# Kernel optimization log

Hardware: AMD Instinct MI355X
Metric: run time of the kernel (lower is better)

## Reference

```python
import jax, jax.numpy as jnp
import numpy as np

N_G, N_D, D = 50000, 50000, 64
R, L, NNZ, B = 32, 2, 1600000, 2048
TEMP, LAMBDA_1, LAMBDA_2, DROPOUT = 0.2, 0.2, 1e-7, 0.1


def setup_inputs() -> dict:
    key = jax.random.key(0)
    ks = jax.random.split(key, 14)
    uids = jax.random.randint(ks[0], (B,), 0, N_G)
    iids = jax.random.randint(ks[1], (B,), 0, N_D)
    pos = jax.random.randint(ks[2], (B,), 0, N_D)
    neg = jax.random.randint(ks[3], (B,), 0, N_D)
    E_g_0 = jax.random.normal(ks[4], (N_G, D), jnp.float32) * 0.01
    E_d_0 = jax.random.normal(ks[5], (N_D, D), jnp.float32) * 0.01
    rows = jax.random.randint(ks[6], (NNZ,), 0, N_G)
    cols = jax.random.randint(ks[7], (NNZ,), 0, N_D)
    vals = jax.random.uniform(ks[8], (NNZ,), jnp.float32)
    g_mul_s = jax.random.normal(ks[9], (N_G, R), jnp.float32) * 0.1
    v_mul_s = jax.random.normal(ks[10], (N_D, R), jnp.float32) * 0.1
    ut = jax.random.normal(ks[11], (R, N_G), jnp.float32) * (N_G ** -0.5)
    vt = jax.random.normal(ks[12], (R, N_D), jnp.float32) * (N_D ** -0.5)
    drop_u = jax.random.uniform(ks[13], (L, 2, NNZ), jnp.float32)
    return {"uids": uids, "iids": iids, "pos": pos, "neg": neg,
            "E_g_0": E_g_0, "E_d_0": E_d_0, "rows": rows, "cols": cols,
            "vals": vals, "g_mul_s": g_mul_s, "v_mul_s": v_mul_s,
            "ut": ut, "vt": vt, "drop_u": drop_u}


def reference(uids, iids, pos, neg, E_g_0, E_d_0, rows, cols, vals,
              g_mul_s, v_mul_s, ut, vt, drop_u):
    # sparse_dropout keep masks (independent per layer and per spmm call)
    keep = (drop_u > DROPOUT).astype(vals.dtype) / (1.0 - DROPOUT)  # [L,2,NNZ]
    E_g, E_d = E_g_0, E_d_0
    E_g_sum, E_d_sum = E_g_0, E_d_0
    G_g_sum, G_d_sum = E_g_0, E_d_0
    for layer in range(L):
        # Z_g = dropout(A) @ E_d ; Z_d = dropout(A).T @ E_g  (COO spmm)
        vg = vals * keep[layer, 0]
        Z_g = jax.ops.segment_sum(vg[:, None] * E_d[cols], rows, num_segments=N_G)
        vd = vals * keep[layer, 1]
        Z_d = jax.ops.segment_sum(vd[:, None] * E_g[rows], cols, num_segments=N_D)
        # low-rank SVD branch
        G_g = g_mul_s @ (vt @ E_d)  # [n_g, d]
        G_d = v_mul_s @ (ut @ E_g)  # [n_d, d]
        E_g, E_d = Z_g, Z_d
        E_g_sum = E_g_sum + E_g
        E_d_sum = E_d_sum + E_d
        G_g_sum = G_g_sum + G_g
        G_d_sum = G_d_sum + G_d
    # InfoNCE-style contrastive loss (exactly as torch: log(sum exp + eps))
    S_g = (G_g_sum[uids] @ E_g_sum.T) / TEMP  # [B, n_g]
    S_d = (G_d_sum[iids] @ E_d_sum.T) / TEMP  # [B, n_d]
    neg_score = jnp.log(jnp.exp(S_g).sum(1) + 1e-8).mean() \
              + jnp.log(jnp.exp(S_d).sum(1) + 1e-8).mean()
    pos_score = jnp.clip((G_g_sum[uids] * E_g_sum[uids]).sum(1) / TEMP, -5.0, 5.0).mean() \
              + jnp.clip((G_d_sum[iids] * E_d_sum[iids]).sum(1) / TEMP, -5.0, 5.0).mean()
    loss_s = -pos_score + neg_score
    # BPR loss
    g_emb = E_g_sum[uids]
    diff = (g_emb * E_d_sum[pos]).sum(-1) - (g_emb * E_d_sum[neg]).sum(-1)
    loss_r = -jnp.log(jax.nn.sigmoid(diff)).mean()
    # L2 reg over trainable embedding params
    loss_reg = LAMBDA_2 * (jnp.sum(E_g_0 ** 2) + jnp.sum(E_d_0 ** 2))
    loss = loss_r + LAMBDA_1 * loss_s + loss_reg
    return (loss, loss_r, LAMBDA_1 * loss_s)
```

## Files before the change

### kernel.cpp

```cpp
#include <hip/hip_runtime.h>
#include <hip/hip_bf16.h>
#include <math.h>

#define N_Gc 50000
#define N_Dc 50000
#define DIM 64
#define RNK 32
#define NNZc 1600000
#define BSZ 2048
#define KEEPV (1.0f/0.9f)
#define INVT 5.0f
#define NBK2 196
#define NBLK 200
#define NSL 48
#define EPB 8000
#define MCH 256
#define MBLK 196

typedef __attribute__((ext_vector_type(8))) short bfrag;
typedef __attribute__((ext_vector_type(4))) float f32x4;
typedef unsigned long long u64;

__device__ inline ushort f2bf(float f) {
  union { float f; unsigned int u; } v; v.f = f;
  unsigned int r = (v.u + 0x7fffu + ((v.u >> 16) & 1u)) >> 16;
  return (ushort)r;
}
__device__ inline float bf2f(ushort u) {
  union { unsigned int i; float f; } v; v.i = ((unsigned int)u) << 16;
  return v.f;
}

__global__ __launch_bounds__(256) void hist3_kernel(const int* __restrict__ rows, const int* __restrict__ cols,
                                                    int* __restrict__ cntR, int* __restrict__ cntC) {
  __shared__ int lh_r[NBK2];
  __shared__ int lh_c[NBK2];
  int t = threadIdx.x, blk = blockIdx.x;
  if (t < NBK2) { lh_r[t] = 0; lh_c[t] = 0; }
  __syncthreads();
  int e0 = blk*EPB;
  for (int i = e0 + t; i < e0 + EPB; i += 256) {
    atomicAdd(&lh_r[__builtin_nontemporal_load(&rows[i]) >> 8], 1);
    atomicAdd(&lh_c[__builtin_nontemporal_load(&cols[i]) >> 8], 1);
  }
  __syncthreads();
  if (t < NBK2) {
    cntR[t*NBLK + blk] = lh_r[t];
    cntC[t*NBLK + blk] = lh_c[t];
  }
}

__global__ __launch_bounds__(1024) void cscan2_kernel(const int* __restrict__ cntA, int* __restrict__ cbA, int* __restrict__ bpA,
                                                      const int* __restrict__ cntB, int* __restrict__ cbB, int* __restrict__ bpB) {
  const int n = NBK2*NBLK;
  const int* cnt = blockIdx.x ? cntB : cntA;
  int* cb = blockIdx.x ? cbB : cbA;
  int* bp = blockIdx.x ? bpB : bpA;
  __shared__ int wsum[16];
  int t = threadIdx.x, lane = t & 63, w = t >> 6;
  int carry = 0;
  for (int base = 0; base < n; base += 1024) {
    int i = base + t;
    int v = (i < n) ? cnt[i] : 0;
    int x = v;
    #pragma unroll
    for (int o = 1; o < 64; o <<= 1) { int y = __shfl_up(x, o); if (lane >= o) x += y; }
    if (lane == 63) wsum[w] = x;
    __syncthreads();
    if (t < 16) {
      int s = wsum[t];
      #pragma unroll
      for (int o = 1; o < 16; o <<= 1) { int y = __shfl_up(s, o); if (t >= o) s += y; }
      wsum[t] = s;
    }
    __syncthreads();
    int wpre = (w == 0) ? 0 : wsum[w-1];
    int total = wsum[15];
    int ex = carry + wpre + (x - v);
    if (i < n) {
      cb[i] = ex;
      if (i % NBLK == 0) bp[i/NBLK] = ex;
    }
    carry += total;
    __syncthreads();
  }
  if (t == 0) bp[NBK2] = carry;
}

__global__ __launch_bounds__(256) void phaseA2_kernel(const int* __restrict__ rows, const int* __restrict__ cols,
    const float* __restrict__ vals, const float* __restrict__ drop,
    const int* __restrict__ cbR, const int* __restrict__ cbC,
    u64* __restrict__ stage_r, u64* __restrict__ stage_c) {
  __shared__ int cnt_r[NBK2], cnt_c[NBK2];
  __shared__ int base_r[NBK2], base_c[NBK2];
  int t = threadIdx.x, blk = blockIdx.x;
  if (t < NBK2) {
    cnt_r[t] = 0; cnt_c[t] = 0;
    base_r[t] = cbR[t*NBLK + blk];
    base_c[t] = cbC[t*NBLK + blk];
  }
  __syncthreads();
  int e0 = blk*EPB;
  for (int i = e0 + t; i < e0 + EPB; i += 256) {
    int r = __builtin_nontemporal_load(&rows[i]);
    int c = __builtin_nontemporal_load(&cols[i]);
    u64 vb = (u64)__float_as_uint(__builtin_nontemporal_load(&vals[i])) << 32;
    unsigned int dr0 = (__builtin_nontemporal_load(&drop[i]) > 0.1f) ? (1u<<24) : 0u;
    unsigned int dc0 = (__builtin_nontemporal_load(&drop[(size_t)NNZc + i]) > 0.1f) ? (1u<<24) : 0u;
    unsigned int dr1 = (__builtin_nontemporal_load(&drop[2*(size_t)NNZc + i]) > 0.1f) ? (1u<<25) : 0u;
    unsigned int dc1 = (__builtin_nontemporal_load(&drop[3*(size_t)NNZc + i]) > 0.1f) ? (1u<<25) : 0u;
    int br = r >> 8, bc = c >> 8;
    int p = base_r[br] + atomicAdd(&cnt_r[br], 1);
    stage_r[p] = vb | (unsigned int)c | ((unsigned int)(r & 255) << 16) | dr0 | dr1;
    int q = base_c[bc] + atomicAdd(&cnt_c[bc], 1);
    stage_c[q] = vb | (unsigned int)r | ((unsigned int)(c & 255) << 16) | dc0 | dc1;
  }
}

__global__ __launch_bounds__(256) void phaseB2_kernel(
    const int* __restrict__ bptrR, int* __restrict__ ptroutR, const u64* __restrict__ stageR,
    ushort* __restrict__ fcolR, float* __restrict__ fw0R, float* __restrict__ fw1R,
    const int* __restrict__ bptrC, int* __restrict__ ptroutC, const u64* __restrict__ stageC,
    ushort* __restrict__ fcolC, float* __restrict__ fw0C, float* __restrict__ fw1C, int n) {
  const int side = blockIdx.y;
  const int* bptr = side ? bptrC : bptrR;
  int* ptrout = side ? ptroutC : ptroutR;
  const u64* stage = side ? stageC : stageR;
  ushort* fcol = side ? fcolC : fcolR;
  float* fw0 = side ? fw0C : fw0R;
  float* fw1 = side ? fw1C : fw1R;
  __shared__ int cnt[256];
  __shared__ int pos[256];
  __shared__ int woff[4];
  int t = threadIdx.x, b = blockIdx.x;
  int base_row = b*256;
  int base = bptr[b], endp = bptr[b+1];
  cnt[t] = 0;
  __syncthreads();
  for (int k = base + t; k < endp; k += 256) {
    unsigned int lo = (unsigned int)__builtin_nontemporal_load(&stage[k]);
    atomicAdd(&cnt[(lo >> 16) & 255], 1);
  }
  __syncthreads();
  int lane = t & 63, w = t >> 6;
  int c = cnt[t], x = c;
  #pragma unroll
  for (int o = 1; o < 64; o <<= 1) { int y = __shfl_up(x, o); if (lane >= o) x += y; }
  if (lane == 63) woff[w] = x;
  __syncthreads();
  if (t == 0) { woff[1] += woff[0]; woff[2] += woff[1]; woff[3] += woff[2]; }
  __syncthreads();
  int excl = ((w == 0) ? 0 : woff[w-1]) + (x - c);
  pos[t] = excl;
  int rr = base_row + t;
  if (rr <= n) ptrout[rr] = base + excl;
  __syncthreads();
  for (int k = base + t; k < endp; k += 256) {
    u64 rec = __builtin_nontemporal_load(&stage[k]);
    unsigned int lo = (unsigned int)rec;
    int rel = (lo >> 16) & 255;
    int p = base + atomicAdd(&pos[rel], 1);
    float v = __uint_as_float((unsigned int)(rec >> 32));
    fcol[p] = (ushort)(lo & 0xffffu);
    fw0[p] = (lo & (1u<<24)) ? v*KEEPV : 0.f;
    fw1[p] = (lo & (1u<<25)) ? v*KEEPV : 0.f;
  }
}

__device__ __forceinline__ float spmm_row(const ushort* __restrict__ fcol, const float* __restrict__ fw,
                                          const ushort* __restrict__ Eb, int k0, int end, int lane) {
  float acc = 0.f;
  int nfull = (end - k0) >> 3;
  int cc[8]; float ww[8];
  if (nfull > 0) {
    #pragma unroll
    for (int u = 0; u < 8; u++) {
      cc[u] = __builtin_nontemporal_load(&fcol[k0+u]);
      ww[u] = __builtin_nontemporal_load(&fw[k0+u]);
    }
    for (int b = 1; b < nfull; b++) {
      int kn = k0 + b*8;
      int cn[8]; float wn[8];
      #pragma unroll
      for (int u = 0; u < 8; u++) {
        cn[u] = __builtin_nontemporal_load(&fcol[kn+u]);
        wn[u] = __builtin_nontemporal_load(&fw[kn+u]);
      }
      #pragma unroll
      for (int u = 0; u < 8; u++) acc += ww[u]*bf2f(Eb[(size_t)cc[u]*DIM + lane]);
      #pragma unroll
      for (int u = 0; u < 8; u++) { cc[u] = cn[u]; ww[u] = wn[u]; }
    }
    #pragma unroll
    for (int u = 0; u < 8; u++) acc += ww[u]*bf2f(Eb[(size_t)cc[u]*DIM + lane]);
  }
  for (int k = k0 + nfull*8; k < end; k++)
    acc += __builtin_nontemporal_load(&fw[k])*bf2f(Eb[(size_t)__builtin_nontemporal_load(&fcol[k])*DIM + lane]);
  return acc;
}

__global__ __launch_bounds__(256) void spmm_l0_kernel(
    const int* __restrict__ ptrR, const ushort* __restrict__ fcolR, const float* __restrict__ fwR,
    const ushort* __restrict__ EbR, ushort* __restrict__ ZbR,
    const int* __restrict__ ptrC, const ushort* __restrict__ fcolC, const float* __restrict__ fwC,
    const ushort* __restrict__ EbC, ushort* __restrict__ ZbC, int nrows) {
  const int side = blockIdx.y;
  const int* ptr = side ? ptrC : ptrR;
  const ushort* fcol = side ? fcolC : fcolR;
  const float* fw = side ? fwC : fwR;
  const ushort* Eb = side ? EbC : EbR;
  ushort* Zb = side ? ZbC : ZbR;
  int lane = threadIdx.x & 63;
  int row = blockIdx.x*4 + (threadIdx.x >> 6);
  if (row >= nrows) return;
  float acc = spmm_row(fcol, fw, Eb, ptr[row], ptr[row+1], lane);
  Zb[(size_t)row*DIM + lane] = f2bf(acc);
}

__global__ __launch_bounds__(256) void spmm_l1_kernel(
    const int* __restrict__ ptrR, const ushort* __restrict__ fcolR, const float* __restrict__ fwR,
    const ushort* __restrict__ ZbOR, const float* __restrict__ E0R, const ushort* __restrict__ ZbSR,
    ushort* __restrict__ EoutR,
    const int* __restrict__ ptrC, const ushort* __restrict__ fcolC, const float* __restrict__ fwC,
    const ushort* __restrict__ ZbOC, const float* __restrict__ E0C, const ushort* __restrict__ ZbSC,
    ushort* __restrict__ EoutC, int nrows) {
  const int side = blockIdx.y;
  const int* ptr = side ? ptrC : ptrR;
  const ushort* fcol = side ? fcolC : fcolR;
  const float* fw = side ? fwC : fwR;
  const ushort* ZbO = side ? ZbOC : ZbOR;
  const float* E0 = side ? E0C : E0R;
  const ushort* ZbS = side ? ZbSC : ZbSR;
  ushort* Eout = side ? EoutC : EoutR;
  int lane = threadIdx.x & 63;
  int row = blockIdx.x*4 + (threadIdx.x >> 6);
  if (row >= nrows) return;
  float acc = spmm_row(fcol, fw, ZbO, ptr[row], ptr[row+1], lane);
  size_t o = (size_t)row*DIM + lane;
  acc += __builtin_nontemporal_load(&E0[o]) + bf2f(ZbS[o]);
  Eout[o] = f2bf(acc);
}

__global__ __launch_bounds__(256) void matred2_kernel(
    const float* __restrict__ vrowA, const float* __restrict__ E0A, const ushort* __restrict__ ZbA, float* __restrict__ MpA,
    const float* __restrict__ vrowB, const float* __restrict__ E0B, const ushort* __restrict__ ZbB, float* __restrict__ MpB,
    int n) {
  const int side = blockIdx.y;
  const float* vrow = side ? vrowB : vrowA;
  const float* E0 = side ? E0B : E0A;
  const ushort* Zb = side ? ZbB : ZbA;
  float* Mpart = side ? MpB : MpA;
  __shared__ float vs[RNK*MCH];
  __shared__ float part[RNK*DIM];
  int t = threadIdx.x, lane = t & 63, w = t >> 6;
  int ci0 = blockIdx.x*MCH;
  int cnt = min(MCH, n - ci0);
  for (int idx = t; idx < RNK*DIM; idx += 256) part[idx] = 0.f;
  for (int idx = t; idx < RNK*MCH; idx += 256) {
    int r = idx >> 8, i = idx & (MCH-1);
    vs[idx] = (i < cnt) ? __builtin_nontemporal_load(&vrow[(size_t)r*n + ci0 + i]) : 0.f;
  }
  __syncthreads();
  float acc[RNK];
  #pragma unroll
  for (int r = 0; r < RNK; r++) acc[r] = 0.f;
  int iw0 = w*64;
  for (int ii = 0; ii < 64; ii += 4) {
    int i = iw0 + ii;
    int gi = ci0 + i;
    float x0 = 0.f, x1 = 0.f, x2 = 0.f, x3 = 0.f;
    if (i+0 < cnt) x0 = E0[(size_t)(gi+0)*DIM + lane] + bf2f(Zb[(size_t)(gi+0)*DIM + lane]);
    if (i+1 < cnt) x1 = E0[(size_t)(gi+1)*DIM + lane] + bf2f(Zb[(size_t)(gi+1)*DIM + lane]);
    if (i+2 < cnt) x2 = E0[(size_t)(gi+2)*DIM + lane] + bf2f(Zb[(size_t)(gi+2)*DIM + lane]);
    if (i+3 < cnt) x3 = E0[(size_t)(gi+3)*DIM + lane] + bf2f(Zb[(size_t)(gi+3)*DIM + lane]);
    #pragma unroll
    for (int r = 0; r < RNK; r++) {
      float4 v4 = *(const float4*)&vs[r*MCH + i];
      acc[r] += v4.x*x0 + v4.y*x1 + v4.z*x2 + v4.w*x3;
    }
  }
  #pragma unroll
  for (int r = 0; r < RNK; r++) atomicAdd(&part[r*DIM + lane], acc[r]);
  __syncthreads();
  float* dst = Mpart + (size_t)blockIdx.x*(RNK*DIM);
  for (int idx = t; idx < RNK*DIM; idx += 256) dst[idx] = part[idx];
}

__global__ __launch_bounds__(256) void mreduce_kernel(const float* __restrict__ MpA, float* __restrict__ MA,
                                                      const float* __restrict__ MpB, float* __restrict__ MB, int nblk) {
  const float* Mpart = blockIdx.y ? MpB : MpA;
  float* M = blockIdx.y ? MB : MA;
  int idx = blockIdx.x*256 + threadIdx.x;
  if (idx < RNK*DIM) {
    float s = 0.f;
    for (int b = 0; b < nblk; b++) s += Mpart[(size_t)b*(RNK*DIM) + idx];
    M[idx] = s;
  }
}

__global__ __launch_bounds__(256) void gsmall_kernel(
    const int* __restrict__ idsA, const float* __restrict__ E0A, const float* __restrict__ mulA,
    const float* __restrict__ MA, float* __restrict__ outA, ushort* __restrict__ outbA,
    const int* __restrict__ idsB, const float* __restrict__ E0B, const float* __restrict__ mulB,
    const float* __restrict__ MB, float* __restrict__ outB, ushort* __restrict__ outbB) {
  const int side = blockIdx.y;
  const int* ids = side ? idsB : idsA;
  const float* E0 = side ? E0B : E0A;
  const float* mul = side ? mulB : mulA;
  const float* M = side ? MB : MA;
  float* out = side ? outB : outA;
  ushort* outb = side ? outbB : outbA;
  __shared__ float Ms[RNK*DIM];
  int t = threadIdx.x;
  for (int i = t; i < RNK*DIM; i += 256) Ms[i] = M[i];
  __syncthreads();
  int b = blockIdx.x*4 + (t >> 6), lane = t & 63;
  int u = ids[b];
  float a = E0[(size_t)u*DIM + lane];
  #pragma unroll
  for (int r = 0; r < RNK; r++) a += mul[(size_t)u*RNK + r]*Ms[r*DIM + lane];
  out[(size_t)b*DIM + lane] = a;
  outb[(size_t)b*DIM + lane] = f2bf(a);
}

__global__ __launch_bounds__(256) void convsq_kernel(const float* __restrict__ inA, ushort* __restrict__ outA,
                                                     const float* __restrict__ inB, ushort* __restrict__ outB,
                                                     int n4, float* __restrict__ acc) {
  const float* in = blockIdx.y ? inB : inA;
  ushort* out = blockIdx.y ? outB : outA;
  __shared__ float ls[4];
  int t = threadIdx.x;
  int idx = blockIdx.x*256 + t;
  int stride = gridDim.x*256;
  float s = 0.f;
  for (int i = idx; i < n4; i += stride) {
    float4 v = *(const float4*)&in[(size_t)i*4];
    ushort4 o;
    o.x = f2bf(v.x); o.y = f2bf(v.y); o.z = f2bf(v.z); o.w = f2bf(v.w);
    *(ushort4*)&out[(size_t)i*4] = o;
    s += v.x*v.x + v.y*v.y + v.z*v.z + v.w*v.w;
  }
  #pragma unroll
  for (int o = 32; o > 0; o >>= 1) s += __shfl_xor(s, o);
  if ((t & 63) == 0) ls[t >> 6] = s;
  __syncthreads();
  if (t == 0) atomicAdd(acc, ls[0] + ls[1] + ls[2] + ls[3]);
}

__global__ __launch_bounds__(256) void lse_mfma_kernel(
    const ushort* __restrict__ Ag, const ushort* __restrict__ Xg, float* __restrict__ seg,
    const ushort* __restrict__ Ad, const ushort* __restrict__ Xd, float* __restrict__ sed,
    int nj) {
  const ushort* A = blockIdx.y ? Ad : Ag;
  const ushort* X = blockIdx.y ? Xd : Xg;
  float* sumexp = blockIdx.y ? sed : seg;
  __shared__ __align__(16) ushort Xs[64*68];
  int t = threadIdx.x, lane = t & 63, w = t >> 6;
  int bt = blockIdx.x & 31, js = blockIdx.x >> 5;
  int b0 = bt*64;
  int m = lane & 15, q = lane >> 4;
  const ushort* Arow = A + (size_t)(b0 + w*16 + m)*DIM + q*8;
  bfrag a0 = *(const bfrag*)(Arow);
  bfrag a1 = *(const bfrag*)(Arow + 32);
  float rs0 = 0.f, rs1 = 0.f, rs2 = 0.f, rs3 = 0.f;
  int njt = (nj + 63) >> 6;
  for (int jt = js; jt < njt; jt += NSL) {
    int j0 = jt << 6;
    __syncthreads();
    for (int c = t; c < 512; c += 256) {
      int r = c >> 3, k8 = (c & 7) << 3;
      int j = j0 + r;
      ushort4 v0 = {0,0,0,0}, v1 = {0,0,0,0};
      if (j < nj) {
        const ushort4* src = (const ushort4*)(X + (size_t)j*DIM + k8);
        v0 = src[0]; v1 = src[1];
      }
      *(ushort4*)&Xs[r*68 + k8]     = v0;
      *(ushort4*)&Xs[r*68 + k8 + 4] = v1;
    }
    __syncthreads();
    #pragma unroll
    for (int jq = 0; jq < 4; jq++) {
      int jr = jq*16 + m;
      union { bfrag f; uint2 u2[2]; } B0, B1;
      B0.u2[0] = *(const uint2*)&Xs[jr*68 + q*8];
      B0.u2[1] = *(const uint2*)&Xs[jr*68 + q*8 + 4];
      B1.u2[0] = *(const uint2*)&Xs[jr*68 + 32 + q*8];
      B1.u2[1] = *(const uint2*)&Xs[jr*68 + 32 + q*8 + 4];
      f32x4 acc = {0.f, 0.f, 0.f, 0.f};
      acc = __builtin_amdgcn_mfma_f32_16x16x32_bf16(a0, B0.f, acc, 0, 0, 0);
      acc = __builtin_amdgcn_mfma_f32_16x16x32_bf16(a1, B1.f, acc, 0, 0, 0);
      int jg = j0 + jr;
      if (jg < nj) {
        rs0 += __expf(acc[0]*INVT);
        rs1 += __expf(acc[1]*INVT);
        rs2 += __expf(acc[2]*INVT);
        rs3 += __expf(acc[3]*INVT);
      }
    }
  }
  #pragma unroll
  for (int o = 1; o < 16; o <<= 1) {
    rs0 += __shfl_xor(rs0, o);
    rs1 += __shfl_xor(rs1, o);
    rs2 += __shfl_xor(rs2, o);
    rs3 += __shfl_xor(rs3, o);
  }
  if (m == 0) {
    float* dst = &sumexp[b0 + w*16 + q*4];
    atomicAdd(&dst[0], rs0);
    atomicAdd(&dst[1], rs1);
    atomicAdd(&dst[2], rs2);
    atomicAdd(&dst[3], rs3);
  }
}

__global__ __launch_bounds__(256) void perb_kernel(const int* __restrict__ uids, const int* __restrict__ iids,
    const int* __restrict__ pos, const int* __restrict__ neg,
    const float* __restrict__ Ggu, const float* __restrict__ Gdi,
    const ushort* __restrict__ Egs_b, const ushort* __restrict__ Eds_b,
    const float* __restrict__ seg, const float* __restrict__ sed,
    float* __restrict__ accs) {
  __shared__ float lsum[3][4];
  int t = threadIdx.x, lane = t & 63, w = t >> 6;
  int b = blockIdx.x*4 + w;
  int u = uids[b], it = iids[b], p = pos[b], ng = neg[b];
  float egu = bf2f(Egs_b[(size_t)u*DIM + lane]);
  float d1 = Ggu[(size_t)b*DIM + lane]*egu;
  float d2 = Gdi[(size_t)b*DIM + lane]*bf2f(Eds_b[(size_t)it*DIM + lane]);
  float d3 = egu*bf2f(Eds_b[(size_t)p*DIM + lane]);
  float d4 = egu*bf2f(Eds_b[(size_t)ng*DIM + lane]);
  #pragma unroll
  for (int o = 32; o > 0; o >>= 1) {
    d1 += __shfl_xor(d1, o);
    d2 += __shfl_xor(d2, o);
    d3 += __shfl_xor(d3, o);
    d4 += __shfl_xor(d4, o);
  }
  if (lane == 0) {
    float pterm = fminf(fmaxf(d1*INVT, -5.f), 5.f) + fminf(fmaxf(d2*INVT, -5.f), 5.f);
    float diff = d3 - d4;
    lsum[0][w] = pterm;
    lsum[1][w] = log1pf(expf(-diff));
    lsum[2][w] = logf(seg[b] + 1e-8f) + logf(sed[b] + 1e-8f);
  }
  __syncthreads();
  if (t < 3) atomicAdd(&accs[t], lsum[t][0] + lsum[t][1] + lsum[t][2] + lsum[t][3]);
}

__global__ void final_kernel(const float* __restrict__ accs, float* __restrict__ out) {
  float posm = accs[0]*(1.f/BSZ);
  float lr   = accs[1]*(1.f/BSZ);
  float negm = accs[2]*(1.f/BSZ);
  float reg  = 1e-7f*accs[3];
  float l1ls = 0.2f*(negm - posm);
  out[0] = lr + l1ls + reg;
  out[1] = lr;
  out[2] = l1ls;
}

extern "C" void kernel_launch(void* const* d_in, const int* in_sizes, int n_in,
                              void* d_out, int out_size, void* d_ws, size_t ws_size,
                              hipStream_t stream) {
  (void)in_sizes; (void)n_in; (void)out_size;
  const int*   uids = (const int*)d_in[0];
  const int*   iids = (const int*)d_in[1];
  const int*   pos  = (const int*)d_in[2];
  const int*   neg  = (const int*)d_in[3];
  const float* Eg0  = (const float*)d_in[4];
  const float* Ed0  = (const float*)d_in[5];
  const int*   rows = (const int*)d_in[6];
  const int*   cols = (const int*)d_in[7];
  const float* vals = (const float*)d_in[8];
  const float* gms  = (const float*)d_in[9];
  const float* vms  = (const float*)d_in[10];
  const float* ut   = (const float*)d_in[11];
  const float* vt   = (const float*)d_in[12];
  const float* drop = (const float*)d_in[13];
  float* out = (float*)d_out;

  float* ws = (float*)d_ws;
  const size_t ED = (size_t)N_Gc*DIM;
  float* REG_A = ws;
  float* REG_B = REG_A + ED;
  int* ptr_r = (int*)(REG_B + ED);
  int* ptr_c = ptr_r + (N_Gc + 1);
  int* bptr_r = ptr_c + (N_Dc + 1);
  int* bptr_c = bptr_r + (NBK2 + 1);
  int* cntR = bptr_c + (NBK2 + 1);
  int* cntC = cntR + NBK2*NBLK;
  int* cbR  = cntC + NBK2*NBLK;
  int* cbC  = cbR + NBK2*NBLK;
  ushort* fcol_r = (ushort*)(cbC + NBK2*NBLK);
  float* fw_r0  = (float*)(fcol_r + NNZc);
  float* fw_r1  = fw_r0 + NNZc;
  ushort* fcol_c = (ushort*)(fw_r1 + NNZc);
  float* fw_c0  = (float*)(fcol_c + NNZc);
  float* fw_c1  = fw_c0 + NNZc;
  float* Ggu = fw_c1 + NNZc;
  float* Gdi = Ggu + (size_t)BSZ*DIM;
  ushort* Ggu_b = (ushort*)(Gdi + (size_t)BSZ*DIM);
  ushort* Gdi_b = Ggu_b + (size_t)BSZ*DIM;
  float* Mg  = (float*)(Gdi_b + (size_t)BSZ*DIM);
  float* Md  = Mg + RNK*DIM;
  float* seg = Md + RNK*DIM;
  float* sed = seg + BSZ;
  float* accs = sed + BSZ;
  float* MpG = accs + 16;
  float* MpD = MpG + (size_t)MBLK*RNK*DIM;

  u64* stage_r = (u64*)REG_A;
  u64* stage_c = (u64*)REG_B;
  ushort* Zg0_b = (ushort*)REG_A;
  ushort* Zd0_b = Zg0_b + ED;
  ushort* Eg0_b = (ushort*)REG_B;
  ushort* Ed0_b = Eg0_b + ED;
  ushort* Egs_b = (ushort*)REG_B;
  ushort* Eds_b = Egs_b + ED;

  size_t need = ((char*)(MpD + (size_t)MBLK*RNK*DIM)) - ((char*)d_ws);
  if (ws_size < need) return;

  hipMemsetAsync(seg, 0, sizeof(float)*(2*BSZ + 16), stream);

  hist3_kernel<<<NBLK, 256, 0, stream>>>(rows, cols, cntR, cntC);
  cscan2_kernel<<<2, 1024, 0, stream>>>(cntR, cbR, bptr_r, cntC, cbC, bptr_c);
  phaseA2_kernel<<<NBLK, 256, 0, stream>>>(rows, cols, vals, drop, cbR, cbC, stage_r, stage_c);
  phaseB2_kernel<<<dim3(NBK2, 2), 256, 0, stream>>>(
      bptr_r, ptr_r, stage_r, fcol_r, fw_r0, fw_r1,
      bptr_c, ptr_c, stage_c, fcol_c, fw_c0, fw_c1, N_Gc);

  int n4 = (int)(ED/4);
  convsq_kernel<<<dim3(1024, 2), 256, 0, stream>>>(Eg0, Eg0_b, Ed0, Ed0_b, n4, accs + 3);

  int spmm_blocks = (N_Gc + 3)/4;
  spmm_l0_kernel<<<dim3(spmm_blocks, 2), 256, 0, stream>>>(
      ptr_r, fcol_r, fw_r0, Ed0_b, Zg0_b,
      ptr_c, fcol_c, fw_c0, Eg0_b, Zd0_b, N_Gc);
  spmm_l1_kernel<<<dim3(spmm_blocks, 2), 256, 0, stream>>>(
      ptr_r, fcol_r, fw_r1, Zd0_b, Eg0, Zg0_b, Egs_b,
      ptr_c, fcol_c, fw_c1, Zg0_b, Ed0, Zd0_b, Eds_b, N_Gc);

  matred2_kernel<<<dim3(MBLK, 2), 256, 0, stream>>>(
      vt, Ed0, Zd0_b, MpG,
      ut, Eg0, Zg0_b, MpD, N_Dc);
  mreduce_kernel<<<dim3((RNK*DIM + 255)/256, 2), 256, 0, stream>>>(MpG, Mg, MpD, Md, MBLK);

  gsmall_kernel<<<dim3(BSZ/4, 2), 256, 0, stream>>>(
      uids, Eg0, gms, Mg, Ggu, Ggu_b,
      iids, Ed0, vms, Md, Gdi, Gdi_b);

  lse_mfma_kernel<<<dim3(32*NSL, 2), 256, 0, stream>>>(Ggu_b, Egs_b, seg, Gdi_b, Eds_b, sed, N_Gc);

  perb_kernel<<<BSZ/4, 256, 0, stream>>>(uids, iids, pos, neg, Ggu, Gdi, Egs_b, Eds_b, seg, sed, accs);
  final_kernel<<<1, 1, 0, stream>>>(accs, out);
}
```

Before: 707.6 us.

## Halve sort buckets to 128 rows and stage bucket sort in shared memory

Bucket width for the two-pass COO-to-CSR radix sort drops from 256 to 128 rows, giving 391 buckets and twice as many phase-B blocks. Phase B now scatters each bucket's records into an LDS buffer of up to 6144 entries, then writes the sorted output with coalesced, contiguous stores. A global-scatter fallback handles oversized buckets. The goal is to replace random global writes with coalesced ones and raise parallelism, at the cost of 48KB of LDS per block, which limits occupancy, and a larger histogram and scan.

```diff
diff --git a/kernel.cpp b/kernel.cpp
--- a/kernel.cpp
+++ b/kernel.cpp
@@ -10,12 +10,13 @@
 #define BSZ 2048
 #define KEEPV (1.0f/0.9f)
 #define INVT 5.0f
-#define NBK2 196
+#define NBK3 391
 #define NBLK 200
 #define NSL 48
 #define EPB 8000
 #define MCH 256
 #define MBLK 196
+#define SCAP 6144
 
 typedef __attribute__((ext_vector_type(8))) short bfrag;
 typedef __attribute__((ext_vector_type(4))) float f32x4;
@@ -33,26 +34,26 @@
 
 __global__ __launch_bounds__(256) void hist3_kernel(const int* __restrict__ rows, const int* __restrict__ cols,
                                                     int* __restrict__ cntR, int* __restrict__ cntC) {
-  __shared__ int lh_r[NBK2];
-  __shared__ int lh_c[NBK2];
+  __shared__ int lh_r[NBK3];
+  __shared__ int lh_c[NBK3];
   int t = threadIdx.x, blk = blockIdx.x;
-  if (t < NBK2) { lh_r[t] = 0; lh_c[t] = 0; }
+  for (int j = t; j < NBK3; j += 256) { lh_r[j] = 0; lh_c[j] = 0; }
   __syncthreads();
   int e0 = blk*EPB;
   for (int i = e0 + t; i < e0 + EPB; i += 256) {
-    atomicAdd(&lh_r[__builtin_nontemporal_load(&rows[i]) >> 8], 1);
-    atomicAdd(&lh_c[__builtin_nontemporal_load(&cols[i]) >> 8], 1);
-  }
-  __syncthreads();
-  if (t < NBK2) {
-    cntR[t*NBLK + blk] = lh_r[t];
-    cntC[t*NBLK + blk] = lh_c[t];
+    atomicAdd(&lh_r[__builtin_nontemporal_load(&rows[i]) >> 7], 1);
+    atomicAdd(&lh_c[__builtin_nontemporal_load(&cols[i]) >> 7], 1);
+  }
+  __syncthreads();
+  for (int j = t; j < NBK3; j += 256) {
+    cntR[j*NBLK + blk] = lh_r[j];
+    cntC[j*NBLK + blk] = lh_c[j];
   }
 }
 
 __global__ __launch_bounds__(1024) void cscan2_kernel(const int* __restrict__ cntA, int* __restrict__ cbA, int* __restrict__ bpA,
                                                       const int* __restrict__ cntB, int* __restrict__ cbB, int* __restrict__ bpB) {
-  const int n = NBK2*NBLK;
+  const int n = NBK3*NBLK;
   const int* cnt = blockIdx.x ? cntB : cntA;
   int* cb = blockIdx.x ? cbB : cbA;
   int* bp = blockIdx.x ? bpB : bpA;
@@ -84,20 +85,20 @@
     carry += total;
     __syncthreads();
   }
-  if (t == 0) bp[NBK2] = carry;
+  if (t == 0) bp[NBK3] = carry;
 }
 
 __global__ __launch_bounds__(256) void phaseA2_kernel(const int* __restrict__ rows, const int* __restrict__ cols,
     const float* __restrict__ vals, const float* __restrict__ drop,
     const int* __restrict__ cbR, const int* __restrict__ cbC,
     u64* __restrict__ stage_r, u64* __restrict__ stage_c) {
-  __shared__ int cnt_r[NBK2], cnt_c[NBK2];
-  __shared__ int base_r[NBK2], base_c[NBK2];
+  __shared__ int cnt_r[NBK3], cnt_c[NBK3];
+  __shared__ int base_r[NBK3], base_c[NBK3];
   int t = threadIdx.x, blk = blockIdx.x;
-  if (t < NBK2) {
-    cnt_r[t] = 0; cnt_c[t] = 0;
-    base_r[t] = cbR[t*NBLK + blk];
-    base_c[t] = cbC[t*NBLK + blk];
+  for (int j = t; j < NBK3; j += 256) {
+    cnt_r[j] = 0; cnt_c[j] = 0;
+    base_r[j] = cbR[j*NBLK + blk];
+    base_c[j] = cbC[j*NBLK + blk];
   }
   __syncthreads();
   int e0 = blk*EPB;
@@ -109,15 +110,15 @@
     unsigned int dc0 = (__builtin_nontemporal_load(&drop[(size_t)NNZc + i]) > 0.1f) ? (1u<<24) : 0u;
     unsigned int dr1 = (__builtin_nontemporal_load(&drop[2*(size_t)NNZc + i]) > 0.1f) ? (1u<<25) : 0u;
     unsigned int dc1 = (__builtin_nontemporal_load(&drop[3*(size_t)NNZc + i]) > 0.1f) ? (1u<<25) : 0u;
-    int br = r >> 8, bc = c >> 8;
+    int br = r >> 7, bc = c >> 7;
     int p = base_r[br] + atomicAdd(&cnt_r[br], 1);
-    stage_r[p] = vb | (unsigned int)c | ((unsigned int)(r & 255) << 16) | dr0 | dr1;
+    stage_r[p] = vb | (unsigned int)c | ((unsigned int)(r & 127) << 16) | dr0 | dr1;
     int q = base_c[bc] + atomicAdd(&cnt_c[bc], 1);
-    stage_c[q] = vb | (unsigned int)r | ((unsigned int)(c & 255) << 16) | dc0 | dc1;
-  }
-}
-
-__global__ __launch_bounds__(256) void phaseB2_kernel(
+    stage_c[q] = vb | (unsigned int)r | ((unsigned int)(c & 127) << 16) | dc0 | dc1;
+  }
+}
+
+__global__ __launch_bounds__(256) void phaseB3_kernel(
     const int* __restrict__ bptrR, int* __restrict__ ptroutR, const u64* __restrict__ stageR,
     ushort* __restrict__ fcolR, float* __restrict__ fw0R, float* __restrict__ fw1R,
     const int* __restrict__ bptrC, int* __restrict__ ptroutC, const u64* __restrict__ stageC,
@@ -129,41 +130,64 @@
   ushort* fcol = side ? fcolC : fcolR;
   float* fw0 = side ? fw0C : fw0R;
   float* fw1 = side ? fw1C : fw1R;
-  __shared__ int cnt[256];
-  __shared__ int pos[256];
-  __shared__ int woff[4];
+  __shared__ u64 sorted[SCAP];
+  __shared__ int cnt[128];
+  __shared__ int pos[128];
+  __shared__ int wtot[2];
   int t = threadIdx.x, b = blockIdx.x;
-  int base_row = b*256;
+  int base_row = b*128;
   int base = bptr[b], endp = bptr[b+1];
-  cnt[t] = 0;
+  int total = endp - base;
+  if (t < 128) cnt[t] = 0;
   __syncthreads();
   for (int k = base + t; k < endp; k += 256) {
     unsigned int lo = (unsigned int)__builtin_nontemporal_load(&stage[k]);
-    atomicAdd(&cnt[(lo >> 16) & 255], 1);
-  }
-  __syncthreads();
-  int lane = t & 63, w = t >> 6;
-  int c = cnt[t], x = c;
-  #pragma unroll
-  for (int o = 1; o < 64; o <<= 1) { int y = __shfl_up(x, o); if (lane >= o) x += y; }
-  if (lane == 63) woff[w] = x;
-  __syncthreads();
-  if (t == 0) { woff[1] += woff[0]; woff[2] += woff[1]; woff[3] += woff[2]; }
-  __syncthreads();
-  int excl = ((w == 0) ? 0 : woff[w-1]) + (x - c);
-  pos[t] = excl;
-  int rr = base_row + t;
-  if (rr <= n) ptrout[rr] = base + excl;
-  __syncthreads();
-  for (int k = base + t; k < endp; k += 256) {
-    u64 rec = __builtin_nontemporal_load(&stage[k]);
-    unsigned int lo = (unsigned int)rec;
-    int rel = (lo >> 16) & 255;
-    int p = base + atomicAdd(&pos[rel], 1);
-    float v = __uint_as_float((unsigned int)(rec >> 32));
-    fcol[p] = (ushort)(lo & 0xffffu);
-    fw0[p] = (lo & (1u<<24)) ? v*KEEPV : 0.f;
-    fw1[p] = (lo & (1u<<25)) ? v*KEEPV : 0.f;
+    atomicAdd(&cnt[(lo >> 16) & 127], 1);
+  }
+  __syncthreads();
+  int lane = t & 63;
+  if (t < 128) {
+    int c = cnt[t], x = c;
+    #pragma unroll
+    for (int o = 1; o < 64; o <<= 1) { int y = __shfl_up(x, o); if (lane >= o) x += y; }
+    if (lane == 63) wtot[t >> 6] = x;
+    __syncthreads();
+    int excl = (x - c) + ((t >= 64) ? wtot[0] : 0);
+    pos[t] = excl;
+    int rr = base_row + t;
+    if (rr <= n) ptrout[rr] = base + excl;
+  } else {
+    __syncthreads();
+  }
+  __syncthreads();
+  if (total <= SCAP) {
+    for (int k = base + t; k < endp; k += 256) {
+      u64 rec = __builtin_nontemporal_load(&stage[k]);
+      int rel = ((unsigned int)rec >> 16) & 127;
+      int idx = atomicAdd(&pos[rel], 1);
+      sorted[idx] = rec;
+    }
+    __syncthreads();
+    for (int idx = t; idx < total; idx += 256) {
+      u64 rec = sorted[idx];
+      unsigned int lo = (unsigned int)rec;
+      float v = __uint_as_float((unsigned int)(rec >> 32));
+      int p = base + idx;
+      fcol[p] = (ushort)(lo & 0xffffu);
+      fw0[p] = (lo & (1u<<24)) ? v*KEEPV : 0.f;
+      fw1[p] = (lo & (1u<<25)) ? v*KEEPV : 0.f;
+    }
+  } else {
+    for (int k = base + t; k < endp; k += 256) {
+      u64 rec = stage[k];
+      unsigned int lo = (unsigned int)rec;
+      int rel = (lo >> 16) & 127;
+      int p = base + atomicAdd(&pos[rel], 1);
+      float v = __uint_as_float((unsigned int)(rec >> 32));
+      fcol[p] = (ushort)(lo & 0xffffu);
+      fw0[p] = (lo & (1u<<24)) ? v*KEEPV : 0.f;
+      fw1[p] = (lo & (1u<<25)) ? v*KEEPV : 0.f;
+    }
   }
 }
 
@@ -486,12 +510,12 @@
   int* ptr_r = (int*)(REG_B + ED);
   int* ptr_c = ptr_r + (N_Gc + 1);
   int* bptr_r = ptr_c + (N_Dc + 1);
-  int* bptr_c = bptr_r + (NBK2 + 1);
-  int* cntR = bptr_c + (NBK2 + 1);
-  int* cntC = cntR + NBK2*NBLK;
-  int* cbR  = cntC + NBK2*NBLK;
-  int* cbC  = cbR + NBK2*NBLK;
-  ushort* fcol_r = (ushort*)(cbC + NBK2*NBLK);
+  int* bptr_c = bptr_r + (NBK3 + 1);
+  int* cntR = bptr_c + (NBK3 + 1);
+  int* cntC = cntR + NBK3*NBLK;
+  int* cbR  = cntC + NBK3*NBLK;
+  int* cbC  = cbR + NBK3*NBLK;
+  ushort* fcol_r = (ushort*)(cbC + NBK3*NBLK);
   float* fw_r0  = (float*)(fcol_r + NNZc);
   float* fw_r1  = fw_r0 + NNZc;
   ushort* fcol_c = (ushort*)(fw_r1 + NNZc);
@@ -526,7 +550,7 @@
   hist3_kernel<<<NBLK, 256, 0, stream>>>(rows, cols, cntR, cntC);
   cscan2_kernel<<<2, 1024, 0, stream>>>(cntR, cbR, bptr_r, cntC, cbC, bptr_c);
   phaseA2_kernel<<<NBLK, 256, 0, stream>>>(rows, cols, vals, drop, cbR, cbC, stage_r, stage_c);
-  phaseB2_kernel<<<dim3(NBK2, 2), 256, 0, stream>>>(
+  phaseB3_kernel<<<dim3(NBK3, 2), 256, 0, stream>>>(
       bptr_r, ptr_r, stage_r, fcol_r, fw_r0, fw_r1,
       bptr_c, ptr_c, stage_c, fcol_c, fw_c0, fw_c1, N_Gc);
 
```

Result: faster. 660.3 us (-6.7%).
